# Optimization experiments

Measured on AMD Instinct MI355X. Metric: run time of the kernel, lower is better.

The kernel has to match this reference:

```python
import jax, jax.numpy as jnp
import numpy as np

DIM = 256; INNER = 512; HEADS = 8; DHEAD = 64; WS = 7; K = 3; EPS = 1e-5

def _rel_idx(ws):
    idx = np.array([[x, y] for x in range(ws) for y in range(ws)])
    d = idx[None, :, :] - idx[:, None, :]
    d[:, :, 0] += ws - 1
    d[:, :, 1] += ws - 1
    d[:, :, 0] *= 2 * ws - 1
    return jnp.asarray(d.sum(-1))  # [ws^2, ws^2] int

REL_IDX = _rel_idx(WS)

def _proj(x, dw, g, b, m, v, pw):
    # depthwise conv (k=3, pad=1, groups=C) -> BN (eval mode) -> 1x1 pointwise
    p = K // 2
    y = jax.lax.conv_general_dilated(x, dw, (1, 1), ((p, p), (p, p)),
                                     feature_group_count=x.shape[1])
    y = (y - m[None, :, None, None]) * jax.lax.rsqrt(v[None, :, None, None] + EPS) \
        * g[None, :, None, None] + b[None, :, None, None]
    return jax.lax.conv_general_dilated(y, pw, (1, 1), 'VALID')

def _windows(t):
    # [b, h*d, H, W] -> [b, h, nw, ws*ws, d]  (non-shuffle partition)
    b, c, H, W = t.shape
    nh, nw = H // WS, W // WS
    t = t.reshape(b, HEADS, DHEAD, nh, WS, nw, WS)
    t = t.transpose(0, 1, 3, 5, 4, 6, 2)  # b h nh nw ws ws d
    return t.reshape(b, HEADS, nh * nw, WS * WS, DHEAD)

def _unwindows(t, H, W):
    b = t.shape[0]
    nh, nw = H // WS, W // WS
    t = t.reshape(b, HEADS, nh, nw, WS, WS, DHEAD)
    t = t.transpose(0, 1, 6, 2, 4, 3, 5)  # b h d nh ws nw ws
    return t.reshape(b, HEADS * DHEAD, H, W)

def setup_inputs() -> dict:
    key = jax.random.key(0)
    ks = jax.random.split(key, 32)
    d = {'x': jax.random.normal(ks[0], (16, DIM, 56, 56), jnp.float32)}
    i = 1
    for p in ('q', 'k', 'v'):
        d[p + '_dw'] = jax.random.normal(ks[i], (DIM, 1, K, K), jnp.float32) * 0.1; i += 1
        d[p + '_g'] = jax.random.uniform(ks[i], (DIM,), jnp.float32); i += 1
        d[p + '_b'] = jax.random.normal(ks[i], (DIM,), jnp.float32) * 0.1; i += 1
        d[p + '_m'] = jax.random.normal(ks[i], (DIM,), jnp.float32) * 0.1; i += 1
        d[p + '_v'] = jax.random.uniform(ks[i], (DIM,), jnp.float32); i += 1
        d[p + '_pw'] = jax.random.normal(ks[i], (INNER, DIM, 1, 1), jnp.float32) * 0.05; i += 1
    d['pos_emb'] = jax.random.normal(ks[i], ((2 * WS - 1) ** 2, HEADS), jnp.float32); i += 1
    d['out_w'] = jax.random.normal(ks[i], (DIM, INNER, 1, 1), jnp.float32) * 0.05; i += 1
    d['out_b'] = jax.random.normal(ks[i], (DIM,), jnp.float32) * 0.1
    return d

def reference(x, q_dw, q_g, q_b, q_m, q_v, q_pw,
              k_dw, k_g, k_b, k_m, k_v, k_pw,
              v_dw, v_g, v_b, v_m, v_v, v_pw,
              pos_emb, out_w, out_b):
    H, W = x.shape[2], x.shape[3]
    q = _windows(_proj(x, q_dw, q_g, q_b, q_m, q_v, q_pw))
    k = _windows(_proj(x, k_dw, k_g, k_b, k_m, k_v, k_pw))
    v = _windows(_proj(x, v_dw, v_g, v_b, v_m, v_v, v_pw))
    dots = jnp.einsum('bhwid,bhwjd->bhwij', q, k) * (DHEAD ** -0.5)
    bias = pos_emb[REL_IDX]              # [i, j, heads]
    dots = dots + bias.transpose(2, 0, 1)[None, :, None]  # broadcast over b, w
    attn = jax.nn.softmax(dots, axis=-1)
    out = jnp.einsum('bhwij,bhwjd->bhwid', attn, v)
    out = _unwindows(out, H, W)
    out = jax.lax.conv_general_dilated(out, out_w, (1, 1), 'VALID') \
          + out_b[None, :, None, None]
    return out
```

## Files before the change

kernel.cpp:

```cpp
#include <hip/hip_runtime.h>
#include <hip/hip_bf16.h>

typedef __hip_bfloat16 bf16;
typedef __bf16 bfv8 __attribute__((ext_vector_type(8)));
typedef float f32x4 __attribute__((ext_vector_type(4)));

constexpr int B_     = 16;
constexpr int C_     = 256;
constexpr int INNER_ = 512;
constexpr int HEADS_ = 8;
constexpr int DH_    = 64;
constexpr int HW_    = 56;
constexpr int NPIX_  = HW_ * HW_;
constexpr int WS_    = 7;
constexpr int WSQ_   = 49;
constexpr int NWIN_  = 64;

static __device__ __forceinline__ void async16(const void* g, void* l) {
    __builtin_amdgcn_global_load_lds(
        (const __attribute__((address_space(1))) unsigned int*)g,
        (__attribute__((address_space(3))) unsigned int*)l, 16, 0, 0);
}

__global__ __launch_bounds__(256) void setup_kernel(
    const float* __restrict__ pw0, const float* __restrict__ pw1,
    const float* __restrict__ pw2, const float* __restrict__ pw3,
    bf16* __restrict__ wq,
    const float* __restrict__ dw0, const float* __restrict__ g0,
    const float* __restrict__ b0, const float* __restrict__ m0,
    const float* __restrict__ v0,
    const float* __restrict__ dw1, const float* __restrict__ g1,
    const float* __restrict__ b1, const float* __restrict__ m1,
    const float* __restrict__ v1,
    const float* __restrict__ dw2, const float* __restrict__ g2,
    const float* __restrict__ b2, const float* __restrict__ m2,
    const float* __restrict__ v2,
    float* __restrict__ wf,
    const float* __restrict__ pos, float* __restrict__ biasf) {
    int bx = blockIdx.x;
    if (bx < 2048) {
        int g = bx >> 9;
        const float* s = g == 0 ? pw0 : (g == 1 ? pw1 : (g == 2 ? pw2 : pw3));
        int i = (bx & 511) * 256 + threadIdx.x;
        wq[(size_t)g * (INNER_ * C_) + i] = __float2bfloat16(s[i]);
    } else if (bx < 2051) {
        int p = bx - 2048, c = threadIdx.x;
        const float* dw = p == 0 ? dw0 : (p == 1 ? dw1 : dw2);
        const float* g  = p == 0 ? g0  : (p == 1 ? g1  : g2);
        const float* bb = p == 0 ? b0  : (p == 1 ? b1  : b2);
        const float* mm = p == 0 ? m0  : (p == 1 ? m1  : m2);
        const float* vv = p == 0 ? v0  : (p == 1 ? v1  : v2);
        float s = g[c] * rsqrtf(vv[c] + 1e-5f);
        float* o = wf + (size_t)(p * 256 + c) * 12;
#pragma unroll
        for (int k = 0; k < 9; ++k) o[k] = dw[c * 9 + k] * s;
        o[9] = bb[c] - mm[c] * s;
        o[10] = 0.f; o[11] = 0.f;
    } else {
        int h = bx - 2051;
        int wv = threadIdx.x >> 6, lane = threadIdx.x & 63;
        int quad = lane >> 4, col16 = lane & 15;
        float* dst = biasf + (((size_t)h * 4 + wv) * 64 + lane) * 16;
#pragma unroll
        for (int nt = 0; nt < 4; ++nt)
#pragma unroll
            for (int r = 0; r < 4; ++r) {
                int row = wv * 16 + quad * 4 + r;
                int col = nt * 16 + col16;
                float v;
                if (col >= WSQ_) v = -1e30f;
                else if (row >= WSQ_) v = 0.f;
                else {
                    int xi = row / WS_, yi = row % WS_;
                    int xj = col / WS_, yj = col % WS_;
                    int rel = (xj - xi + 6) * 13 + (yj - yi + 6);
                    v = pos[rel * HEADS_ + h];
                }
                dst[nt * 4 + r] = v;
            }
    }
}

__global__ __launch_bounds__(256) void dwbn3_kernel(
    const float* __restrict__ x, const float* __restrict__ wf,
    bf16* __restrict__ tq, bf16* __restrict__ tk, bf16* __restrict__ tv) {
    __shared__ float xs[3 * 64 * 61];
    int y  = blockIdx.x;
    int c0 = blockIdx.y * 64;
    int b  = blockIdx.z;
    int tid = threadIdx.x;
    for (int i = tid; i < 2688; i += 256) {
        int row = i / 896;
        int rem = i - row * 896;
        int ch = rem / 14, s = rem - ch * 14;
        int yy = y + row - 1;
        float4 v4 = make_float4(0.f, 0.f, 0.f, 0.f);
        if (yy >= 0 && yy < HW_)
            v4 = *(const float4*)(x + (size_t)(b * C_ + c0 + ch) * NPIX_
                                    + yy * HW_ + s * 4);
        float* d = xs + (row * 64 + ch) * 61 + 1 + s * 4;
        d[0] = v4.x; d[1] = v4.y; d[2] = v4.z; d[3] = v4.w;
    }
    for (int j = tid; j < 192; j += 256) {
        int row = j >> 6, ch = j & 63;
        xs[(row * 64 + ch) * 61] = 0.f;
        xs[(row * 64 + ch) * 61 + 57] = 0.f;
    }
    __syncthreads();

    int cg = tid & 31, xo = tid >> 5;
    int bcol = xo * 7;
    unsigned int pack[3][7];
#pragma unroll
    for (int ci = 0; ci < 2; ++ci) {
        int ch = cg * 2 + ci;
        float4 w[3][3];
#pragma unroll
        for (int p = 0; p < 3; ++p) {
            const float* wp = wf + (size_t)(p * 256 + c0 + ch) * 12;
            w[p][0] = *(const float4*)(wp);
            w[p][1] = *(const float4*)(wp + 4);
            w[p][2] = *(const float4*)(wp + 8);
        }
        const float* r0 = xs + ch * 61;
        const float* r1 = r0 + 64 * 61;
        const float* r2 = r1 + 64 * 61;
        float a00 = r0[bcol], a01 = r0[bcol + 1];
        float a10 = r1[bcol], a11 = r1[bcol + 1];
        float a20 = r2[bcol], a21 = r2[bcol + 1];
#pragma unroll
        for (int px = 0; px < 7; ++px) {
            float a02 = r0[bcol + px + 2];
            float a12 = r1[bcol + px + 2];
            float a22 = r2[bcol + px + 2];
#pragma unroll
            for (int p = 0; p < 3; ++p) {
                float acc = w[p][2].y
                    + w[p][0].x * a00 + w[p][0].y * a01 + w[p][0].z * a02
                    + w[p][0].w * a10 + w[p][1].x * a11 + w[p][1].y * a12
                    + w[p][1].z * a20 + w[p][1].w * a21 + w[p][2].x * a22;
                bf16 hv = __float2bfloat16(acc);
                unsigned short u; __builtin_memcpy(&u, &hv, 2);
                if (ci == 0) pack[p][px] = u;
                else         pack[p][px] |= ((unsigned int)u) << 16;
            }
            a00 = a01; a01 = a02; a10 = a11; a11 = a12; a20 = a21; a21 = a22;
        }
    }
    bf16* outs[3] = {tq, tk, tv};
    size_t pbase = ((size_t)b * NPIX_ + y * HW_ + bcol) * C_ + c0 + cg * 2;
#pragma unroll
    for (int p = 0; p < 3; ++p)
#pragma unroll
        for (int px = 0; px < 7; ++px)
            *(unsigned int*)(outs[p] + pbase + px * C_) = pack[p][px];
}

__global__ __launch_bounds__(256) void gemm_qkv_mfma(
    const bf16* __restrict__ Wbase, const bf16* __restrict__ Tbase,
    bf16* __restrict__ Qbase) {
    __shared__ __align__(16) char smem[128 * 136 * 2];
    bf16* sA = (bf16*)smem;
    bf16* sB = sA + 128 * 32;
    bf16* sC = (bf16*)smem;
    int tid = threadIdx.x;
    int lin = blockIdx.x + (blockIdx.y << 2) + blockIdx.z * 100;
    int s  = lin & 7;
    int u  = lin >> 3;
    int ch_t = u & 3;
    int v  = u >> 2;
    int pz = v * 8 + s;
    int pix_t = pz % 25;
    int z     = pz / 25;
    int zp = z >> 4;
    int b  = z & 15;
    int c0 = ch_t * 128;
    int p0 = pix_t * 128;
    const bf16* W = Wbase + (size_t)zp * (INNER_ * C_);
    const bf16* T = Tbase + (size_t)zp * ((size_t)B_ * NPIX_ * C_);
    bf16* Q = Qbase + (size_t)zp * ((size_t)B_ * INNER_ * NPIX_);
    float qscale = (zp == 0) ? 0.125f : 1.0f;

    int row0 = tid >> 2;
    int kc   = (tid & 3) * 8;
    int pA0 = p0 + row0;       if (pA0 > NPIX_ - 1) pA0 = NPIX_ - 1;
    int pA1 = p0 + row0 + 64;  if (pA1 > NPIX_ - 1) pA1 = NPIX_ - 1;
    const bf16* gA0 = T + ((size_t)b * NPIX_ + pA0) * 256 + kc;
    const bf16* gA1 = T + ((size_t)b * NPIX_ + pA1) * 256 + kc;
    const bf16* gB0 = W + (size_t)(c0 + row0) * 256 + kc;
    const bf16* gB1 = W + (size_t)(c0 + row0 + 64) * 256 + kc;
    char* lA = (char*)sA + tid * 16;
    char* lB = (char*)sB + tid * 16;

    int lane = tid & 63, wv = tid >> 6;
    int wm = (wv >> 1) * 64;
    int wn = (wv & 1) * 64;
    int col16 = lane & 15, quad = lane >> 4;

    f32x4 acc[4][4] = {};
    for (int k0 = 0; k0 < 256; k0 += 32) {
        async16(gA0, lA);
        async16(gA1, lA + 4096);
        async16(gB0, lB);
        async16(gB1, lB + 4096);
        gA0 += 32; gA1 += 32; gB0 += 32; gB1 += 32;
        __syncthreads();
        bfv8 af[4], bfr[4];
#pragma unroll
        for (int mt = 0; mt < 4; ++mt)
            af[mt] = *(const bfv8*)(sA + (wm + mt * 16 + col16) * 32 + quad * 8);
#pragma unroll
        for (int nt = 0; nt < 4; ++nt)
            bfr[nt] = *(const bfv8*)(sB + (wn + nt * 16 + col16) * 32 + quad * 8);
#pragma unroll
        for (int mt = 0; mt < 4; ++mt)
#pragma unroll
            for (int nt = 0; nt < 4; ++nt)
                acc[mt][nt] = __builtin_amdgcn_mfma_f32_16x16x32_bf16(
                    af[mt], bfr[nt], acc[mt][nt], 0, 0, 0);
        __syncthreads();
    }
#pragma unroll
    for (int mt = 0; mt < 4; ++mt)
#pragma unroll
        for (int nt = 0; nt < 4; ++nt) {
            f32x4 a = acc[mt][nt];
#pragma unroll
            for (int r = 0; r < 4; ++r)
                sC[(wm + mt * 16 + quad * 4 + r) * 136 + wn + nt * 16 + col16] =
                    __float2bfloat16(a[r] * qscale);
        }
    __syncthreads();
#pragma unroll
    for (int j = 0; j < 8; ++j) {
        int lin2 = j * 256 + tid;
        int pixl = lin2 >> 4, chg = lin2 & 15;
        int p = p0 + pixl;
        if (p < NPIX_) {
            int ch = c0 + chg * 8;
            int h = ch >> 6, d = ch & 63;
            int yy = p / HW_, xx = p % HW_;
            int wdw = (yy / WS_) * 8 + (xx / WS_);
            int j49 = (yy % WS_) * WS_ + (xx % WS_);
            bfv8 vd = *(const bfv8*)(sC + pixl * 136 + chg * 8);
            *(bfv8*)(Q + ((((size_t)b * HEADS_ + h) * NWIN_ + wdw) * WSQ_ + j49) * DH_ + d) = vd;
        }
    }
}

__global__ __launch_bounds__(256) void attn_mfma(
    const bf16* __restrict__ Q, const bf16* __restrict__ Kt,
    const bf16* __restrict__ V, const float* __restrict__ biasf,
    bf16* __restrict__ O) {
    __shared__ __align__(16) bf16 qs[64 * 72];
    __shared__ __align__(16) bf16 ks[64 * 72];
    __shared__ __align__(16) bf16 vt[64 * 72];
    bf16* ps = qs;
    int tid = threadIdx.x;
    int w = blockIdx.x & 63;
    int h = (blockIdx.x >> 6) & 7;
    int b = blockIdx.x >> 9;
    size_t base = (((size_t)b * HEADS_ + h) * NWIN_ + w) * (WSQ_ * DH_);

    {
        bfv8 z = {};
#pragma unroll
        for (int it = 0; it < 2; ++it) {
            int c = it * 256 + tid;
            int row = c >> 3, col = (c & 7) * 8;
            bfv8 vq = z, vk = z;
            if (c < 392) {
                vq = *(const bfv8*)(Q + base + c * 8);
                vk = *(const bfv8*)(Kt + base + c * 8);
            }
            *(bfv8*)(qs + row * 72 + col) = vq;
            *(bfv8*)(ks + row * 72 + col) = vk;
        }
#pragma unroll
        for (int it = 0; it < 2; ++it) {
            int idx = it * 256 + tid;
            int d = idx & 63, j8 = idx >> 6;
            bf16 val[8];
            if (j8 < 6) {
#pragma unroll
                for (int u = 0; u < 8; ++u)
                    val[u] = V[base + (j8 * 8 + u) * 64 + d];
            } else {
#pragma unroll
                for (int u = 0; u < 8; ++u) {
                    int j = j8 * 8 + u;
                    val[u] = (j < WSQ_) ? V[base + j * 64 + d]
                                        : __float2bfloat16(0.f);
                }
            }
            *(bfv8*)(vt + d * 72 + j8 * 8) = *(const bfv8*)val;
        }
    }
    __syncthreads();

    int lane = tid & 63, wv = tid >> 6;
    int band = wv * 16;
    int col16 = lane & 15, quad = lane >> 4;

    bfv8 aq0 = *(const bfv8*)(qs + (band + col16) * 72 + quad * 8);
    bfv8 aq1 = *(const bfv8*)(qs + (band + col16) * 72 + 32 + quad * 8);
    bfv8 bk[4][2];
#pragma unroll
    for (int nt = 0; nt < 4; ++nt) {
        bk[nt][0] = *(const bfv8*)(ks + (nt * 16 + col16) * 72 + quad * 8);
        bk[nt][1] = *(const bfv8*)(ks + (nt * 16 + col16) * 72 + 32 + quad * 8);
    }
    __syncthreads();

    const float* bp = biasf + (((size_t)h * 4 + wv) * 64 + lane) * 16;
    f32x4 sacc[4];
#pragma unroll
    for (int nt = 0; nt < 4; ++nt) {
        sacc[nt] = *(const f32x4*)(bp + nt * 4);
        sacc[nt] = __builtin_amdgcn_mfma_f32_16x16x32_bf16(aq0, bk[nt][0], sacc[nt], 0, 0, 0);
        sacc[nt] = __builtin_amdgcn_mfma_f32_16x16x32_bf16(aq1, bk[nt][1], sacc[nt], 0, 0, 0);
    }
    float p[4][4];
    float inv[4];
#pragma unroll
    for (int r = 0; r < 4; ++r) {
        float s0 = sacc[0][r], s1 = sacc[1][r], s2 = sacc[2][r], s3 = sacc[3][r];
        float mx = fmaxf(fmaxf(s0, s1), fmaxf(s2, s3));
        mx = fmaxf(mx, __shfl_xor(mx, 1, 16));
        mx = fmaxf(mx, __shfl_xor(mx, 2, 16));
        mx = fmaxf(mx, __shfl_xor(mx, 4, 16));
        mx = fmaxf(mx, __shfl_xor(mx, 8, 16));
        float e0 = __expf(s0 - mx), e1 = __expf(s1 - mx);
        float e2 = __expf(s2 - mx), e3 = __expf(s3 - mx);
        float sm = e0 + e1 + e2 + e3;
        sm += __shfl_xor(sm, 1, 16);
        sm += __shfl_xor(sm, 2, 16);
        sm += __shfl_xor(sm, 4, 16);
        sm += __shfl_xor(sm, 8, 16);
        p[0][r] = e0; p[1][r] = e1; p[2][r] = e2; p[3][r] = e3;
        inv[r] = 1.f / sm;
    }
#pragma unroll
    for (int nt = 0; nt < 4; ++nt)
#pragma unroll
        for (int r = 0; r < 4; ++r)
            ps[(band + quad * 4 + r) * 72 + nt * 16 + col16] = __float2bfloat16(p[nt][r]);
    f32x4 oacc[4] = {};
    bfv8 ap0 = *(const bfv8*)(ps + (band + col16) * 72 + quad * 8);
    bfv8 ap1 = *(const bfv8*)(ps + (band + col16) * 72 + 32 + quad * 8);
#pragma unroll
    for (int nt = 0; nt < 4; ++nt) {
        bfv8 bv0 = *(const bfv8*)(vt + (nt * 16 + col16) * 72 + quad * 8);
        bfv8 bv1 = *(const bfv8*)(vt + (nt * 16 + col16) * 72 + 32 + quad * 8);
        oacc[nt] = __builtin_amdgcn_mfma_f32_16x16x32_bf16(ap0, bv0, oacc[nt], 0, 0, 0);
        oacc[nt] = __builtin_amdgcn_mfma_f32_16x16x32_bf16(ap1, bv1, oacc[nt], 0, 0, 0);
    }
    int wy = w >> 3, wx = w & 7;
#pragma unroll
    for (int r = 0; r < 4; ++r) {
        int i = band + quad * 4 + r;
        if (i < WSQ_) {
            int py = wy * WS_ + i / WS_, px = wx * WS_ + i % WS_;
            size_t ob = ((size_t)b * NPIX_ + py * HW_ + px) * INNER_ + h * DH_;
            float sc = inv[r];
#pragma unroll
            for (int nt = 0; nt < 4; ++nt)
                O[ob + nt * 16 + col16] = __float2bfloat16(oacc[nt][r] * sc);
        }
    }
}

__global__ __launch_bounds__(256) void gemm_out_mfma(
    const bf16* __restrict__ W, const bf16* __restrict__ O,
    const float* __restrict__ bias, float* __restrict__ out) {
    __shared__ __align__(16) bf16 sA[128 * 32];
    __shared__ __align__(16) bf16 sB[128 * 32];
    int tid = threadIdx.x;
    int lin = blockIdx.x + (blockIdx.y << 1) + blockIdx.z * 50;
    int s  = lin & 7;
    int u  = lin >> 3;
    int ch_t = u & 1;
    int v  = u >> 1;
    int pz = v * 8 + s;
    int pix_t = pz % 25;
    int b     = pz / 25;
    int c0 = ch_t * 128;
    int p0 = pix_t * 128;

    int row0 = tid >> 2;
    int kc   = (tid & 3) * 8;
    int pB0 = p0 + row0;       if (pB0 > NPIX_ - 1) pB0 = NPIX_ - 1;
    int pB1 = p0 + row0 + 64;  if (pB1 > NPIX_ - 1) pB1 = NPIX_ - 1;
    const bf16* gA0 = W + (size_t)(c0 + row0) * 512 + kc;
    const bf16* gA1 = W + (size_t)(c0 + row0 + 64) * 512 + kc;
    const bf16* gB0 = O + ((size_t)b * NPIX_ + pB0) * 512 + kc;
    const bf16* gB1 = O + ((size_t)b * NPIX_ + pB1) * 512 + kc;
    char* lA = (char*)sA + tid * 16;
    char* lB = (char*)sB + tid * 16;

    int lane = tid & 63, wv = tid >> 6;
    int wm = (wv >> 1) * 64;
    int wn = (wv & 1) * 64;
    int col16 = lane & 15, quad = lane >> 4;

    f32x4 acc[4][4] = {};
    for (int k0 = 0; k0 < 512; k0 += 32) {
        async16(gA0, lA);
        async16(gA1, lA + 4096);
        async16(gB0, lB);
        async16(gB1, lB + 4096);
        gA0 += 32; gA1 += 32; gB0 += 32; gB1 += 32;
        __syncthreads();
        bfv8 af[4], bfr[4];
#pragma unroll
        for (int mt = 0; mt < 4; ++mt)
            af[mt] = *(const bfv8*)(sA + (wm + mt * 16 + col16) * 32 + quad * 8);
#pragma unroll
        for (int nt = 0; nt < 4; ++nt)
            bfr[nt] = *(const bfv8*)(sB + (wn + nt * 16 + col16) * 32 + quad * 8);
#pragma unroll
        for (int mt = 0; mt < 4; ++mt)
#pragma unroll
            for (int nt = 0; nt < 4; ++nt)
                acc[mt][nt] = __builtin_amdgcn_mfma_f32_16x16x32_bf16(
                    af[mt], bfr[nt], acc[mt][nt], 0, 0, 0);
        __syncthreads();
    }
#pragma unroll
    for (int mt = 0; mt < 4; ++mt) {
#pragma unroll
        for (int r = 0; r < 4; ++r) {
            int ch = c0 + wm + mt * 16 + quad * 4 + r;
            float bc = bias[ch];
#pragma unroll
            for (int nt = 0; nt < 4; ++nt) {
                int p = p0 + wn + nt * 16 + col16;
                if (p < NPIX_)
                    out[((size_t)b * C_ + ch) * NPIX_ + p] = acc[mt][nt][r] + bc;
            }
        }
    }
}

extern "C" void kernel_launch(void* const* d_in, const int* in_sizes, int n_in,
                              void* d_out, int out_size, void* d_ws, size_t ws_size,
                              hipStream_t stream) {
    (void)in_sizes; (void)n_in; (void)out_size; (void)ws_size;
    const float* x     = (const float*)d_in[0];
    const float* pos   = (const float*)d_in[19];
    const float* out_w = (const float*)d_in[20];
    const float* out_b = (const float*)d_in[21];

    size_t tElems = (size_t)B_ * NPIX_ * C_;
    size_t qElems = (size_t)B_ * INNER_ * NPIX_;
    bf16* tq = (bf16*)d_ws;
    bf16* q  = tq + 3 * tElems;
    bf16* o  = tq;
    float* wf = (float*)(q + 3 * qElems);
    bf16* wq = (bf16*)(wf + 3 * 256 * 12);
    bf16* wo = wq + 3 * (INNER_ * C_);
    float* biasf = (float*)(wo + C_ * INNER_);

    dim3 blk(256);
    dim3 gDw(HW_, 4, B_);
    dim3 gQkv(4, 25, 48);
    dim3 gOut(2, 25, 16);

    setup_kernel<<<2059, blk, 0, stream>>>(
        (const float*)d_in[6], (const float*)d_in[12], (const float*)d_in[18],
        out_w, wq,
        (const float*)d_in[1],  (const float*)d_in[2],  (const float*)d_in[3],
        (const float*)d_in[4],  (const float*)d_in[5],
        (const float*)d_in[7],  (const float*)d_in[8],  (const float*)d_in[9],
        (const float*)d_in[10], (const float*)d_in[11],
        (const float*)d_in[13], (const float*)d_in[14], (const float*)d_in[15],
        (const float*)d_in[16], (const float*)d_in[17], wf,
        pos, biasf);

    dwbn3_kernel<<<gDw, blk, 0, stream>>>(x, wf, tq, tq + tElems, tq + 2 * tElems);
    gemm_qkv_mfma<<<gQkv, blk, 0, stream>>>(wq, tq, q);
    attn_mfma<<<B_ * HEADS_ * NWIN_, blk, 0, stream>>>(
        q, q + qElems, q + 2 * qElems, biasf, o);
    gemm_out_mfma<<<gOut, blk, 0, stream>>>(wo, o, out_b, (float*)d_out);
}
```

Measured before the change: 336.8 us.

## Fuse windowed attention with output projection, looping heads per window block

After: 445.0 us. 1.32x slower.

```diff
diff --git a/kernel.cpp b/kernel.cpp
--- a/kernel.cpp
+++ b/kernel.cpp
@@ -248,196 +248,156 @@
     }
 }
 
-__global__ __launch_bounds__(256) void attn_mfma(
+__global__ __launch_bounds__(256) void attn_out_mfma(
     const bf16* __restrict__ Q, const bf16* __restrict__ Kt,
     const bf16* __restrict__ V, const float* __restrict__ biasf,
-    bf16* __restrict__ O) {
+    const bf16* __restrict__ Wo, const float* __restrict__ out_b,
+    float* __restrict__ out) {
     __shared__ __align__(16) bf16 qs[64 * 72];
     __shared__ __align__(16) bf16 ks[64 * 72];
     __shared__ __align__(16) bf16 vt[64 * 72];
+    __shared__ __align__(16) bf16 wol[256 * 68];
     bf16* ps = qs;
+    bf16* os = ks;
     int tid = threadIdx.x;
-    int w = blockIdx.x & 63;
-    int h = (blockIdx.x >> 6) & 7;
-    int b = blockIdx.x >> 9;
-    size_t base = (((size_t)b * HEADS_ + h) * NWIN_ + w) * (WSQ_ * DH_);
-
-    {
-        bfv8 z = {};
-#pragma unroll
-        for (int it = 0; it < 2; ++it) {
-            int c = it * 256 + tid;
-            int row = c >> 3, col = (c & 7) * 8;
-            bfv8 vq = z, vk = z;
-            if (c < 392) {
-                vq = *(const bfv8*)(Q + base + c * 8);
-                vk = *(const bfv8*)(Kt + base + c * 8);
-            }
-            *(bfv8*)(qs + row * 72 + col) = vq;
-            *(bfv8*)(ks + row * 72 + col) = vk;
-        }
-#pragma unroll
-        for (int it = 0; it < 2; ++it) {
-            int idx = it * 256 + tid;
-            int d = idx & 63, j8 = idx >> 6;
-            bf16 val[8];
-            if (j8 < 6) {
-#pragma unroll
-                for (int u = 0; u < 8; ++u)
-                    val[u] = V[base + (j8 * 8 + u) * 64 + d];
-            } else {
-#pragma unroll
-                for (int u = 0; u < 8; ++u) {
-                    int j = j8 * 8 + u;
-                    val[u] = (j < WSQ_) ? V[base + j * 64 + d]
-                                        : __float2bfloat16(0.f);
-                }
-            }
-            *(bfv8*)(vt + d * 72 + j8 * 8) = *(const bfv8*)val;
-        }
-    }
-    __syncthreads();
+    int bx = blockIdx.x;
+    int wx = bx >> 7;
+    int b  = (bx >> 3) & 15;
+    int wy = bx & 7;
+    int w  = wy * 8 + wx;
 
     int lane = tid & 63, wv = tid >> 6;
     int band = wv * 16;
     int col16 = lane & 15, quad = lane >> 4;
 
-    bfv8 aq0 = *(const bfv8*)(qs + (band + col16) * 72 + quad * 8);
-    bfv8 aq1 = *(const bfv8*)(qs + (band + col16) * 72 + 32 + quad * 8);
-    bfv8 bk[4][2];
-#pragma unroll
-    for (int nt = 0; nt < 4; ++nt) {
-        bk[nt][0] = *(const bfv8*)(ks + (nt * 16 + col16) * 72 + quad * 8);
-        bk[nt][1] = *(const bfv8*)(ks + (nt * 16 + col16) * 72 + 32 + quad * 8);
-    }
-    __syncthreads();
-
-    const float* bp = biasf + (((size_t)h * 4 + wv) * 64 + lane) * 16;
-    f32x4 sacc[4];
-#pragma unroll
-    for (int nt = 0; nt < 4; ++nt) {
-        sacc[nt] = *(const f32x4*)(bp + nt * 4);
-        sacc[nt] = __builtin_amdgcn_mfma_f32_16x16x32_bf16(aq0, bk[nt][0], sacc[nt], 0, 0, 0);
-        sacc[nt] = __builtin_amdgcn_mfma_f32_16x16x32_bf16(aq1, bk[nt][1], sacc[nt], 0, 0, 0);
-    }
-    float p[4][4];
-    float inv[4];
-#pragma unroll
-    for (int r = 0; r < 4; ++r) {
-        float s0 = sacc[0][r], s1 = sacc[1][r], s2 = sacc[2][r], s3 = sacc[3][r];
-        float mx = fmaxf(fmaxf(s0, s1), fmaxf(s2, s3));
-        mx = fmaxf(mx, __shfl_xor(mx, 1, 16));
-        mx = fmaxf(mx, __shfl_xor(mx, 2, 16));
-        mx = fmaxf(mx, __shfl_xor(mx, 4, 16));
-        mx = fmaxf(mx, __shfl_xor(mx, 8, 16));
-        float e0 = __expf(s0 - mx), e1 = __expf(s1 - mx);
-        float e2 = __expf(s2 - mx), e3 = __expf(s3 - mx);
-        float sm = e0 + e1 + e2 + e3;
-        sm += __shfl_xor(sm, 1, 16);
-        sm += __shfl_xor(sm, 2, 16);
-        sm += __shfl_xor(sm, 4, 16);
-        sm += __shfl_xor(sm, 8, 16);
-        p[0][r] = e0; p[1][r] = e1; p[2][r] = e2; p[3][r] = e3;
-        inv[r] = 1.f / sm;
-    }
-#pragma unroll
-    for (int nt = 0; nt < 4; ++nt)
-#pragma unroll
-        for (int r = 0; r < 4; ++r)
-            ps[(band + quad * 4 + r) * 72 + nt * 16 + col16] = __float2bfloat16(p[nt][r]);
-    f32x4 oacc[4] = {};
-    bfv8 ap0 = *(const bfv8*)(ps + (band + col16) * 72 + quad * 8);
-    bfv8 ap1 = *(const bfv8*)(ps + (band + col16) * 72 + 32 + quad * 8);
-#pragma unroll
-    for (int nt = 0; nt < 4; ++nt) {
-        bfv8 bv0 = *(const bfv8*)(vt + (nt * 16 + col16) * 72 + quad * 8);
-        bfv8 bv1 = *(const bfv8*)(vt + (nt * 16 + col16) * 72 + 32 + quad * 8);
-        oacc[nt] = __builtin_amdgcn_mfma_f32_16x16x32_bf16(ap0, bv0, oacc[nt], 0, 0, 0);
-        oacc[nt] = __builtin_amdgcn_mfma_f32_16x16x32_bf16(ap1, bv1, oacc[nt], 0, 0, 0);
-    }
-    int wy = w >> 3, wx = w & 7;
+    float bc[16];
+#pragma unroll
+    for (int nt = 0; nt < 16; ++nt) bc[nt] = out_b[nt * 16 + col16];
+
+    f32x4 oacc[16] = {};
+
+    for (int h = 0; h < HEADS_; ++h) {
+        if (h > 0) __syncthreads();
+        size_t base = (((size_t)b * HEADS_ + h) * NWIN_ + w) * (WSQ_ * DH_);
+        {
+            bfv8 z = {};
+#pragma unroll
+            for (int it = 0; it < 2; ++it) {
+                int c = it * 256 + tid;
+                int row = c >> 3, col = (c & 7) * 8;
+                bfv8 vq = z, vk = z;
+                if (c < 392) {
+                    vq = *(const bfv8*)(Q + base + c * 8);
+                    vk = *(const bfv8*)(Kt + base + c * 8);
+                }
+                *(bfv8*)(qs + row * 72 + col) = vq;
+                *(bfv8*)(ks + row * 72 + col) = vk;
+            }
+#pragma unroll
+            for (int it = 0; it < 2; ++it) {
+                int idx = it * 256 + tid;
+                int d = idx & 63, j8 = idx >> 6;
+                bf16 val[8];
+                if (j8 < 6) {
+#pragma unroll
+                    for (int u = 0; u < 8; ++u)
+                        val[u] = V[base + (j8 * 8 + u) * 64 + d];
+                } else {
+#pragma unroll
+                    for (int u = 0; u < 8; ++u) {
+                        int j = j8 * 8 + u;
+                        val[u] = (j < WSQ_) ? V[base + j * 64 + d]
+                                            : __float2bfloat16(0.f);
+                    }
+                }
+                *(bfv8*)(vt + d * 72 + j8 * 8) = *(const bfv8*)val;
+            }
+#pragma unroll
+            for (int it = 0; it < 8; ++it) {
+                int c = it * 256 + tid;
+                int n = c >> 3, k8 = (c & 7) * 8;
+                bfv8 vw = *(const bfv8*)(Wo + (size_t)n * 512 + h * 64 + k8);
+                *(bfv8*)(wol + n * 68 + k8) = vw;
+            }
+        }
+        __syncthreads();
+        bfv8 aq0 = *(const bfv8*)(qs + (band + col16) * 72 + quad * 8);
+        bfv8 aq1 = *(const bfv8*)(qs + (band + col16) * 72 + 32 + quad * 8);
+        bfv8 bk[4][2];
+#pragma unroll
+        for (int nt = 0; nt < 4; ++nt) {
+            bk[nt][0] = *(const bfv8*)(ks + (nt * 16 + col16) * 72 + quad * 8);
+            bk[nt][1] = *(const bfv8*)(ks + (nt * 16 + col16) * 72 + 32 + quad * 8);
+        }
+        __syncthreads();
+
+        const float* bp = biasf + (((size_t)h * 4 + wv) * 64 + lane) * 16;
+        f32x4 sacc[4];
+#pragma unroll
+        for (int nt = 0; nt < 4; ++nt) {
+            sacc[nt] = *(const f32x4*)(bp + nt * 4);
+            sacc[nt] = __builtin_amdgcn_mfma_f32_16x16x32_bf16(aq0, bk[nt][0], sacc[nt], 0, 0, 0);
+            sacc[nt] = __builtin_amdgcn_mfma_f32_16x16x32_bf16(aq1, bk[nt][1], sacc[nt], 0, 0, 0);
+        }
+        float p[4][4], inv[4];
+#pragma unroll
+        for (int r = 0; r < 4; ++r) {
+            float s0 = sacc[0][r], s1 = sacc[1][r], s2 = sacc[2][r], s3 = sacc[3][r];
+            float mx = fmaxf(fmaxf(s0, s1), fmaxf(s2, s3));
+            mx = fmaxf(mx, __shfl_xor(mx, 1, 16));
+            mx = fmaxf(mx, __shfl_xor(mx, 2, 16));
+            mx = fmaxf(mx, __shfl_xor(mx, 4, 16));
+            mx = fmaxf(mx, __shfl_xor(mx, 8, 16));
+            float e0 = __expf(s0 - mx), e1 = __expf(s1 - mx);
+            float e2 = __expf(s2 - mx), e3 = __expf(s3 - mx);
+            float sm = e0 + e1 + e2 + e3;
+            sm += __shfl_xor(sm, 1, 16);
+            sm += __shfl_xor(sm, 2, 16);
+            sm += __shfl_xor(sm, 4, 16);
+            sm += __shfl_xor(sm, 8, 16);
+            p[0][r] = e0; p[1][r] = e1; p[2][r] = e2; p[3][r] = e3;
+            inv[r] = 1.f / sm;
+        }
+#pragma unroll
+        for (int nt = 0; nt < 4; ++nt)
+#pragma unroll
+            for (int r = 0; r < 4; ++r)
+                ps[(band + quad * 4 + r) * 72 + nt * 16 + col16] = __float2bfloat16(p[nt][r]);
+        f32x4 ohacc[4] = {};
+        bfv8 ap0 = *(const bfv8*)(ps + (band + col16) * 72 + quad * 8);
+        bfv8 ap1 = *(const bfv8*)(ps + (band + col16) * 72 + 32 + quad * 8);
+#pragma unroll
+        for (int nt = 0; nt < 4; ++nt) {
+            bfv8 bv0 = *(const bfv8*)(vt + (nt * 16 + col16) * 72 + quad * 8);
+            bfv8 bv1 = *(const bfv8*)(vt + (nt * 16 + col16) * 72 + 32 + quad * 8);
+            ohacc[nt] = __builtin_amdgcn_mfma_f32_16x16x32_bf16(ap0, bv0, ohacc[nt], 0, 0, 0);
+            ohacc[nt] = __builtin_amdgcn_mfma_f32_16x16x32_bf16(ap1, bv1, ohacc[nt], 0, 0, 0);
+        }
+#pragma unroll
+        for (int nt = 0; nt < 4; ++nt)
+#pragma unroll
+            for (int r = 0; r < 4; ++r)
+                os[(band + quad * 4 + r) * 72 + nt * 16 + col16] =
+                    __float2bfloat16(ohacc[nt][r] * inv[r]);
+        bfv8 ao0 = *(const bfv8*)(os + (band + col16) * 72 + quad * 8);
+        bfv8 ao1 = *(const bfv8*)(os + (band + col16) * 72 + 32 + quad * 8);
+#pragma unroll
+        for (int nt = 0; nt < 16; ++nt) {
+            bfv8 bw0 = *(const bfv8*)(wol + (nt * 16 + col16) * 68 + quad * 8);
+            bfv8 bw1 = *(const bfv8*)(wol + (nt * 16 + col16) * 68 + 32 + quad * 8);
+            oacc[nt] = __builtin_amdgcn_mfma_f32_16x16x32_bf16(ao0, bw0, oacc[nt], 0, 0, 0);
+            oacc[nt] = __builtin_amdgcn_mfma_f32_16x16x32_bf16(ao1, bw1, oacc[nt], 0, 0, 0);
+        }
+    }
 #pragma unroll
     for (int r = 0; r < 4; ++r) {
         int i = band + quad * 4 + r;
         if (i < WSQ_) {
-            int py = wy * WS_ + i / WS_, px = wx * WS_ + i % WS_;
-            size_t ob = ((size_t)b * NPIX_ + py * HW_ + px) * INNER_ + h * DH_;
-            float sc = inv[r];
-#pragma unroll
-            for (int nt = 0; nt < 4; ++nt)
-                O[ob + nt * 16 + col16] = __float2bfloat16(oacc[nt][r] * sc);
-        }
-    }
-}
-
-__global__ __launch_bounds__(256) void gemm_out_mfma(
-    const bf16* __restrict__ W, const bf16* __restrict__ O,
-    const float* __restrict__ bias, float* __restrict__ out) {
-    __shared__ __align__(16) bf16 sA[128 * 32];
-    __shared__ __align__(16) bf16 sB[128 * 32];
-    int tid = threadIdx.x;
-    int lin = blockIdx.x + (blockIdx.y << 1) + blockIdx.z * 50;
-    int s  = lin & 7;
-    int u  = lin >> 3;
-    int ch_t = u & 1;
-    int v  = u >> 1;
-    int pz = v * 8 + s;
-    int pix_t = pz % 25;
-    int b     = pz / 25;
-    int c0 = ch_t * 128;
-    int p0 = pix_t * 128;
-
-    int row0 = tid >> 2;
-    int kc   = (tid & 3) * 8;
-    int pB0 = p0 + row0;       if (pB0 > NPIX_ - 1) pB0 = NPIX_ - 1;
-    int pB1 = p0 + row0 + 64;  if (pB1 > NPIX_ - 1) pB1 = NPIX_ - 1;
-    const bf16* gA0 = W + (size_t)(c0 + row0) * 512 + kc;
-    const bf16* gA1 = W + (size_t)(c0 + row0 + 64) * 512 + kc;
-    const bf16* gB0 = O + ((size_t)b * NPIX_ + pB0) * 512 + kc;
-    const bf16* gB1 = O + ((size_t)b * NPIX_ + pB1) * 512 + kc;
-    char* lA = (char*)sA + tid * 16;
-    char* lB = (char*)sB + tid * 16;
-
-    int lane = tid & 63, wv = tid >> 6;
-    int wm = (wv >> 1) * 64;
-    int wn = (wv & 1) * 64;
-    int col16 = lane & 15, quad = lane >> 4;
-
-    f32x4 acc[4][4] = {};
-    for (int k0 = 0; k0 < 512; k0 += 32) {
-        async16(gA0, lA);
-        async16(gA1, lA + 4096);
-        async16(gB0, lB);
-        async16(gB1, lB + 4096);
-        gA0 += 32; gA1 += 32; gB0 += 32; gB1 += 32;
-        __syncthreads();
-        bfv8 af[4], bfr[4];
-#pragma unroll
-        for (int mt = 0; mt < 4; ++mt)
-            af[mt] = *(const bfv8*)(sA + (wm + mt * 16 + col16) * 32 + quad * 8);
-#pragma unroll
-        for (int nt = 0; nt < 4; ++nt)
-            bfr[nt] = *(const bfv8*)(sB + (wn + nt * 16 + col16) * 32 + quad * 8);
-#pragma unroll
-        for (int mt = 0; mt < 4; ++mt)
-#pragma unroll
-            for (int nt = 0; nt < 4; ++nt)
-                acc[mt][nt] = __builtin_amdgcn_mfma_f32_16x16x32_bf16(
-                    af[mt], bfr[nt], acc[mt][nt], 0, 0, 0);
-        __syncthreads();
-    }
-#pragma unroll
-    for (int mt = 0; mt < 4; ++mt) {
-#pragma unroll
-        for (int r = 0; r < 4; ++r) {
-            int ch = c0 + wm + mt * 16 + quad * 4 + r;
-            float bc = bias[ch];
-#pragma unroll
-            for (int nt = 0; nt < 4; ++nt) {
-                int p = p0 + wn + nt * 16 + col16;
-                if (p < NPIX_)
-                    out[((size_t)b * C_ + ch) * NPIX_ + p] = acc[mt][nt][r] + bc;
-            }
+            int pix = (wy * WS_ + i / WS_) * HW_ + wx * WS_ + i % WS_;
+            float* ob = out + (size_t)b * C_ * NPIX_ + pix;
+#pragma unroll
+            for (int nt = 0; nt < 16; ++nt)
+                ob[(size_t)(nt * 16 + col16) * NPIX_] = oacc[nt][r] + bc[nt];
         }
     }
 }
@@ -455,7 +415,6 @@
     size_t qElems = (size_t)B_ * INNER_ * NPIX_;
     bf16* tq = (bf16*)d_ws;
     bf16* q  = tq + 3 * tElems;
-    bf16* o  = tq;
     float* wf = (float*)(q + 3 * qElems);
     bf16* wq = (bf16*)(wf + 3 * 256 * 12);
     bf16* wo = wq + 3 * (INNER_ * C_);
@@ -464,7 +423,6 @@
     dim3 blk(256);
     dim3 gDw(HW_, 4, B_);
     dim3 gQkv(4, 25, 48);
-    dim3 gOut(2, 25, 16);
 
     setup_kernel<<<2059, blk, 0, stream>>>(
         (const float*)d_in[6], (const float*)d_in[12], (const float*)d_in[18],
@@ -479,7 +437,6 @@
 
     dwbn3_kernel<<<gDw, blk, 0, stream>>>(x, wf, tq, tq + tElems, tq + 2 * tElems);
     gemm_qkv_mfma<<<gQkv, blk, 0, stream>>>(wq, tq, q);
-    attn_mfma<<<B_ * HEADS_ * NWIN_, blk, 0, stream>>>(
-        q, q + qElems, q + 2 * qElems, biasf, o);
-    gemm_out_mfma<<<gOut, blk, 0, stream>>>(wo, o, out_b, (float*)d_out);
-}
+    attn_out_mfma<<<B_ * NWIN_, blk, 0, stream>>>(
+        q, q + qElems, q + 2 * qElems, biasf, wo, out_b, (float*)d_out);
+}
```
